# Optimization experiments

Measured on AMD Instinct MI355X. Metric: run time of the kernel, lower is better.

## Reference

```python
import jax, jax.numpy as jnp
import numpy as np

# Int8 fixed-point (power-of-two scale) quant params, mirroring Brevitas
# Int8ActPerTensorFixedPoint / Uint8ActPerTensorFixedPoint with fixed learned scales.
QMAX, QMIN, UQMAX = 127.0, -128.0, 255.0
IO_SCALE = 2.0 ** -4    # io_quant (int8) range ~ [-8, 7.94]
ACC_SCALE = 2.0 ** -3   # gate_acc_quant (int8) range ~ [-16, 15.875]
SIG_SCALE = 2.0 ** -8   # sigmoid_quant (uint8) range [0, ~0.996]
TANH_SCALE = 2.0 ** -7  # tanh_quant (int8) range ~ [-1, 0.992]


def ste_round(x):
    return x + jax.lax.stop_gradient(jnp.round(x) - x)


def qd(x, scale, qmin, qmax):
    # quantize-dequantize with straight-through rounding
    return scale * jnp.clip(ste_round(x / scale), qmin, qmax)


def quant_weight(w):
    # Int8WeightPerTensorFixedPoint: power-of-two per-tensor scale from max-abs stats
    maxabs = jax.lax.stop_gradient(jnp.max(jnp.abs(w)))
    scale = jax.lax.stop_gradient(2.0 ** jnp.ceil(jnp.log2(maxabs / QMAX)))
    return qd(w, scale, QMIN, QMAX)


def setup_inputs() -> dict:
    key = jax.random.key(0)
    ks = jax.random.split(key, 8)
    B, S, V, E, H, O = 64, 512, 32000, 512, 512, 2
    return {
        "text": jax.random.randint(ks[0], (B, S), 0, V, dtype=jnp.int32),
        "text_lengths": jax.random.randint(ks[1], (B,), 1, S, dtype=jnp.int32),
        "emb_w": jax.random.normal(ks[2], (V, E), jnp.float32) * 0.05,
        "w_ih": jax.random.normal(ks[3], (4 * H, E), jnp.float32) * 0.05,
        "w_hh": jax.random.normal(ks[4], (4 * H, H), jnp.float32) * 0.05,
        "b_ih": jax.random.normal(ks[5], (4 * H,), jnp.float32) * 0.05,
        "b_hh": jax.random.normal(ks[6], (4 * H,), jnp.float32) * 0.05,
        "fc_w": jax.random.normal(ks[7], (O, H), jnp.float32) * 0.05,
    }


def reference(text, text_lengths, emb_w, w_ih, w_hh, b_ih, b_hh, fc_w):
    B = text.shape[0]
    H = w_hh.shape[1]

    # quantized embedding lookup + io quant on LSTM input
    x = quant_weight(emb_w)[text]               # [B,S,E]
    x = qd(x, IO_SCALE, QMIN, QMAX)

    wih_q = quant_weight(w_ih)
    whh_q = quant_weight(w_hh)

    # precompute input contribution to gates: [B,S,4H]
    xg = jnp.einsum("bse,ge->bsg", x, wih_q) + b_ih + b_hh

    def step(carry, xg_t):
        h, c = carry
        gates = qd(xg_t + h @ whh_q.T, ACC_SCALE, QMIN, QMAX)  # gate_acc quant
        i, f, g, o = jnp.split(gates, 4, axis=-1)
        i = qd(jax.nn.sigmoid(i), SIG_SCALE, 0.0, UQMAX)
        f = qd(jax.nn.sigmoid(f), SIG_SCALE, 0.0, UQMAX)
        o = qd(jax.nn.sigmoid(o), SIG_SCALE, 0.0, UQMAX)
        g = qd(jnp.tanh(g), TANH_SCALE, QMIN, QMAX)
        c = f * c + i * g
        h = qd(o * qd(jnp.tanh(c), TANH_SCALE, QMIN, QMAX), IO_SCALE, QMIN, QMAX)
        return (h, c), h

    h0 = jnp.zeros((B, H), x.dtype)
    (hT, cT), _ = jax.lax.scan(step, (h0, h0), jnp.swapaxes(xg, 0, 1))

    hidden_state = hT[None]                     # [1,B,H] like torch LSTM
    return hidden_state @ quant_weight(fc_w).T  # [1,B,O]
```

## Files before the change

### kernel.cpp

```cpp
#include <hip/hip_runtime.h>
#include <math.h>

#define S_LEN  512
#define BATCH  64
#define E_DIM  512
#define H_DIM  512
#define G4     2048
#define VOCAB  32000
#define NWG    16

typedef int v4i __attribute__((ext_vector_type(4)));
typedef unsigned long long u64;

#define O_BAR   0
#define O_MAX   256
#define O_H8    512
#define O_FC8   131584
#define O_WIH8  132608
#define O_WHH8  (O_WIH8 + 1048576)
#define O_X8    (O_WHH8 + 1048576)

__device__ __forceinline__ float clampf(float x, float lo, float hi) {
    return fminf(fmaxf(x, lo), hi);
}

__device__ __forceinline__ int scale_exp(float maxabs) {
    double t = (double)maxabs / 127.0;
    int e; double f = frexp(t, &e);
    return (f == 0.5) ? (e - 1) : e;
}

__device__ __forceinline__ float xla_tanhf(float x) {
    if (fabsf(x) < 0.0004f) return x;
    float xc = fminf(fmaxf(x, -7.90531110763549805f), 7.90531110763549805f);
    float x2 = __fmul_rn(xc, xc);
    float p = fmaf(x2, -2.76076847742355e-16f, 2.00018790482477e-13f);
    p = fmaf(x2, p, -8.60467152213735e-11f);
    p = fmaf(x2, p, 5.12229709037114e-08f);
    p = fmaf(x2, p, 1.48572235717979e-05f);
    p = fmaf(x2, p, 6.37261928875436e-04f);
    p = fmaf(x2, p, 4.89352455891786e-03f);
    p = __fmul_rn(xc, p);
    float q = fmaf(x2, 1.19825839466702e-06f, 1.18534705686654e-04f);
    q = fmaf(x2, q, 2.26843463243900e-03f);
    q = fmaf(x2, q, 4.89352518554385e-03f);
    return __fdiv_rn(p, q);
}

__global__ void k_maxabs(const float* __restrict__ x, int n, unsigned* __restrict__ out) {
    unsigned m = 0;
    for (int i = blockIdx.x * blockDim.x + threadIdx.x; i < n; i += gridDim.x * blockDim.x)
        m = max(m, __float_as_uint(fabsf(x[i])));
    #pragma unroll
    for (int o = 32; o > 0; o >>= 1) {
        unsigned other = (unsigned)__shfl_down((int)m, o, 64);
        m = max(m, other);
    }
    __shared__ unsigned sm[4];
    if ((threadIdx.x & 63) == 0) sm[threadIdx.x >> 6] = m;
    __syncthreads();
    if (threadIdx.x == 0) {
        unsigned r = sm[0];
        for (int w = 1; w < (int)(blockDim.x >> 6); w++) r = max(r, sm[w]);
        atomicMax(out, r);
    }
}

__global__ void k_quantw(const float* __restrict__ w, int n, const unsigned* __restrict__ mx,
                         signed char* __restrict__ q) {
    float inv = ldexpf(1.0f, -scale_exp(__uint_as_float(*mx)));
    for (int i = blockIdx.x * blockDim.x + threadIdx.x; i < n; i += gridDim.x * blockDim.x) {
        float v = clampf(rintf(w[i] * inv), -128.0f, 127.0f);
        q[i] = (signed char)(int)v;
    }
}

__global__ void k_embed(const float* __restrict__ emb, const int* __restrict__ text,
                        const unsigned* __restrict__ mx, signed char* __restrict__ x8) {
    int row = blockIdx.x;
    int b = row >> 9, s = row & 511;
    int tok = text[row];
    int ke = scale_exp(__uint_as_float(*mx));
    float inv = ldexpf(1.0f, -ke);
    float sc2 = ldexpf(1.0f, ke + 4);
    const float4* src = (const float4*)(emb + (size_t)tok * E_DIM);
    char4* dst = (char4*)(x8 + (size_t)(s * BATCH + b) * E_DIM);
    float4 v = src[threadIdx.x];
    char4 c;
    float q;
    q = clampf(rintf(v.x * inv), -128.f, 127.f); c.x = (signed char)(int)clampf(rintf(q * sc2), -128.f, 127.f);
    q = clampf(rintf(v.y * inv), -128.f, 127.f); c.y = (signed char)(int)clampf(rintf(q * sc2), -128.f, 127.f);
    q = clampf(rintf(v.z * inv), -128.f, 127.f); c.z = (signed char)(int)clampf(rintf(q * sc2), -128.f, 127.f);
    q = clampf(rintf(v.w * inv), -128.f, 127.f); c.w = (signed char)(int)clampf(rintf(q * sc2), -128.f, 127.f);
    dst[threadIdx.x] = c;
}

#define MKFRAG(a, b) ((v4i){(a)[0], (a)[1], (b)[0], (b)[1]})

__global__ __launch_bounds__(256, 1) void k_lstm(
    const signed char* __restrict__ wih8, const signed char* __restrict__ whh8,
    const signed char* __restrict__ x8, const float* __restrict__ b_ih,
    const float* __restrict__ b_hh, const unsigned* __restrict__ mx,
    signed char* __restrict__ h8) {
    __shared__ __attribute__((aligned(16))) signed char wih_lds[128 * 528];
    __shared__ __attribute__((aligned(16))) signed char hstage[BATCH * 32];
    __shared__ float lut_sig[256];
    __shared__ float lut_tnh[256];

    const int g = blockIdx.x;
    const int tid = threadIdx.x;
    const int wv = tid >> 6, lane = tid & 63, l15 = lane & 15, qd4 = lane >> 4;
    const float sih = ldexpf(1.0f, scale_exp(__uint_as_float(mx[1])) - 4);
    const float shh = ldexpf(1.0f, scale_exp(__uint_as_float(mx[2])) - 4);

    if (tid < 256) {
        float v = (float)(tid - 128) * 0.125f;
        float sg = __fadd_rn(0.5f, __fmul_rn(0.5f, xla_tanhf(__fmul_rn(0.5f, v))));
        float sc = clampf(rintf(__fmul_rn(sg, 256.0f)), 0.0f, 255.0f);
        lut_sig[tid] = sc * 0.00390625f;
        float th = xla_tanhf(v);
        float tc = clampf(rintf(__fmul_rn(th, 128.0f)), -128.0f, 127.0f);
        lut_tnh[tid] = tc * 0.0078125f;
    }

    for (int it = 0; it < 16; it++) {
        int idx = it * 256 + tid;
        int r = idx >> 5, cc = (idx & 31) * 16;
        int grow = (r >> 5) * 512 + g * 32 + (r & 31);
        *(v4i*)(wih_lds + r * 528 + cc) = *(const v4i*)(wih8 + (size_t)grow * 512 + cc);
    }

    v4i whf[8][8];
    #pragma unroll
    for (int nt = 0; nt < 8; nt++) {
        int nl = nt * 16 + l15;
        size_t grow = (size_t)((nl >> 5) * 512 + g * 32 + (nl & 31)) * 512;
        #pragma unroll
        for (int k = 0; k < 8; k++)
            whf[nt][k] = *(const v4i*)(whh8 + grow + k * 64 + qd4 * 16);
    }
    __syncthreads();

    float bi[8], bh[8];
    #pragma unroll
    for (int nt = 0; nt < 8; nt++) {
        int nl = nt * 16 + l15;
        int col = (nl >> 5) * 512 + g * 32 + (nl & 31);
        bi[nt] = b_ih[col];
        bh[nt] = b_hh[col];
    }

    float cst[2][4];
    #pragma unroll
    for (int jh = 0; jh < 2; jh++)
        #pragma unroll
        for (int r = 0; r < 4; r++) cst[jh][r] = 0.0f;

    v4i xacc[8];
    {
        v4i xfr[8];
        const signed char* xrow = x8 + (size_t)(wv * 16 + l15) * 512 + qd4 * 16;
        #pragma unroll
        for (int k = 0; k < 8; k++) xfr[k] = *(const v4i*)(xrow + k * 64);
        #pragma unroll
        for (int nt = 0; nt < 8; nt++) {
            v4i a = (v4i){0, 0, 0, 0};
            #pragma unroll
            for (int k = 0; k < 8; k++) {
                v4i bf = *(const v4i*)(wih_lds + (nt * 16 + l15) * 528 + k * 64 + qd4 * 16);
                a = __builtin_amdgcn_mfma_i32_16x16x64_i8(xfr[k], bf, a, 0, 0, 0);
            }
            xacc[nt] = a;
        }
    }

    const int row = wv * 16 + l15;
    const int pb = tid >> 2, psub = tid & 3;
    const u64 paddr_base = (u64)(h8) + (u64)(pb * 64 + g * 4 + psub) * 16;
    const u64 caddr_base = (u64)(h8) + (u64)(row * 64 + qd4 * 2) * 16;

    for (int t = 0; t < S_LEN; t++) {
        u64 ha = caddr_base + (u64)(t & 1) * 65536;
        int tg = t;
        v4i u0,u1,u2,u3,u4,u5,u6,u7,u8,u9,u10,u11,u12,u13,u14,u15;
        for (;;) {
            asm volatile(
                "global_load_dwordx4 %0,  %16, off sc0 sc1\n\t"
                "global_load_dwordx4 %1,  %16, off offset:16 sc0 sc1\n\t"
                "global_load_dwordx4 %2,  %16, off offset:128 sc0 sc1\n\t"
                "global_load_dwordx4 %3,  %16, off offset:144 sc0 sc1\n\t"
                "global_load_dwordx4 %4,  %16, off offset:256 sc0 sc1\n\t"
                "global_load_dwordx4 %5,  %16, off offset:272 sc0 sc1\n\t"
                "global_load_dwordx4 %6,  %16, off offset:384 sc0 sc1\n\t"
                "global_load_dwordx4 %7,  %16, off offset:400 sc0 sc1\n\t"
                "global_load_dwordx4 %8,  %16, off offset:512 sc0 sc1\n\t"
                "global_load_dwordx4 %9,  %16, off offset:528 sc0 sc1\n\t"
                "global_load_dwordx4 %10, %16, off offset:640 sc0 sc1\n\t"
                "global_load_dwordx4 %11, %16, off offset:656 sc0 sc1\n\t"
                "global_load_dwordx4 %12, %16, off offset:768 sc0 sc1\n\t"
                "global_load_dwordx4 %13, %16, off offset:784 sc0 sc1\n\t"
                "global_load_dwordx4 %14, %16, off offset:896 sc0 sc1\n\t"
                "global_load_dwordx4 %15, %16, off offset:912 sc0 sc1\n\t"
                "s_waitcnt vmcnt(0)"
                : "=&v"(u0), "=&v"(u1), "=&v"(u2), "=&v"(u3),
                  "=&v"(u4), "=&v"(u5), "=&v"(u6), "=&v"(u7),
                  "=&v"(u8), "=&v"(u9), "=&v"(u10), "=&v"(u11),
                  "=&v"(u12), "=&v"(u13), "=&v"(u14), "=&v"(u15)
                : "v"(ha)
                : "memory");
            bool ok = (u0[2] == tg) & (u1[2] == tg) & (u2[2] == tg) & (u3[2] == tg)
                    & (u4[2] == tg) & (u5[2] == tg) & (u6[2] == tg) & (u7[2] == tg)
                    & (u8[2] == tg) & (u9[2] == tg) & (u10[2] == tg) & (u11[2] == tg)
                    & (u12[2] == tg) & (u13[2] == tg) & (u14[2] == tg) & (u15[2] == tg);
            if (ok) break;
            __builtin_amdgcn_s_sleep(1);
        }
        v4i afr[8];
        afr[0] = MKFRAG(u0, u1);   afr[1] = MKFRAG(u2, u3);
        afr[2] = MKFRAG(u4, u5);   afr[3] = MKFRAG(u6, u7);
        afr[4] = MKFRAG(u8, u9);   afr[5] = MKFRAG(u10, u11);
        afr[6] = MKFRAG(u12, u13); afr[7] = MKFRAG(u14, u15);

        float pre[8][4];
        #pragma unroll
        for (int nt = 0; nt < 8; nt++) {
            v4i hacc = (v4i){0, 0, 0, 0};
            #pragma unroll
            for (int k = 0; k < 8; k++)
                hacc = __builtin_amdgcn_mfma_i32_16x16x64_i8(afr[k], whf[nt][k], hacc, 0, 0, 0);
            #pragma unroll
            for (int r = 0; r < 4; r++)
                pre[nt][r] = __fadd_rn(
                    __fadd_rn(__fadd_rn(__fmul_rn((float)xacc[nt][r], sih), bi[nt]), bh[nt]),
                    __fmul_rn((float)hacc[r], shh));
        }

        #pragma unroll
        for (int jh = 0; jh < 2; jh++)
            #pragma unroll
            for (int r = 0; r < 4; r++) {
                int ii = (int)clampf(rintf(__fmul_rn(pre[0 + jh][r], 8.0f)), -128.f, 127.f) + 128;
                int fi = (int)clampf(rintf(__fmul_rn(pre[2 + jh][r], 8.0f)), -128.f, 127.f) + 128;
                int gi = (int)clampf(rintf(__fmul_rn(pre[4 + jh][r], 8.0f)), -128.f, 127.f) + 128;
                int oi = (int)clampf(rintf(__fmul_rn(pre[6 + jh][r], 8.0f)), -128.f, 127.f) + 128;
                float iq = lut_sig[ii], fq = lut_sig[fi], oq = lut_sig[oi];
                float gq = lut_tnh[gi];
                float c = __fadd_rn(__fmul_rn(fq, cst[jh][r]), __fmul_rn(iq, gq));
                cst[jh][r] = c;
                float tc32 = xla_tanhf(c);
                float tq = clampf(rintf(__fmul_rn(tc32, 128.0f)), -128.f, 127.f) * 0.0078125f;
                float hv = __fmul_rn(oq, tq);
                int hc = (int)clampf(rintf(__fmul_rn(hv, 16.0f)), -128.f, 127.f);
                int b = wv * 16 + qd4 * 4 + r;
                hstage[b * 32 + jh * 16 + l15] = (signed char)hc;
            }

        {
            u64 codes = *(const u64*)(hstage + tid * 8);
            v4i sval = (v4i){(int)(codes & 0xffffffffu), (int)(codes >> 32), t + 1, 0};
            u64 pa = paddr_base + (u64)((t + 1) & 1) * 65536;
            asm volatile("global_store_dwordx4 %0, %1, off sc0 sc1"
                         :: "v"(pa), "v"(sval) : "memory");
        }

        if (t + 1 < S_LEN) {
            v4i xfr[8];
            const signed char* xrow = x8 + (size_t)((t + 1) * BATCH + wv * 16 + l15) * 512 + qd4 * 16;
            #pragma unroll
            for (int k = 0; k < 8; k++) xfr[k] = *(const v4i*)(xrow + k * 64);
            #pragma unroll
            for (int nt = 0; nt < 8; nt++) {
                v4i a = (v4i){0, 0, 0, 0};
                #pragma unroll
                for (int k = 0; k < 8; k++) {
                    v4i bf = *(const v4i*)(wih_lds + (nt * 16 + l15) * 528 + k * 64 + qd4 * 16);
                    a = __builtin_amdgcn_mfma_i32_16x16x64_i8(xfr[k], bf, a, 0, 0, 0);
                }
                xacc[nt] = a;
            }
        }
    }
}

__global__ void k_fc(const signed char* __restrict__ h8, const signed char* __restrict__ fc8,
                     const unsigned* __restrict__ mx_fc, float* __restrict__ out) {
    int tid = threadIdx.x;
    int b = tid >> 1, o = tid & 1;
    const signed char* hp = h8 + b * 1024;
    const char4* wp = (const char4*)(fc8 + o * 512);
    int s = 0;
    for (int i = 0; i < 64; i++) {
        u64 hv = __hip_atomic_load((const u64*)(hp + i * 16), __ATOMIC_RELAXED, __HIP_MEMORY_SCOPE_AGENT);
        char4 w0 = wp[i * 2], w1 = wp[i * 2 + 1];
        signed char hb[8];
        *(u64*)hb = hv;
        s += hb[0] * w0.x + hb[1] * w0.y + hb[2] * w0.z + hb[3] * w0.w
           + hb[4] * w1.x + hb[5] * w1.y + hb[6] * w1.z + hb[7] * w1.w;
    }
    float sc = ldexpf(1.0f, scale_exp(__uint_as_float(*mx_fc)) - 4);
    out[b * 2 + o] = (float)s * sc;
}

extern "C" void kernel_launch(void* const* d_in, const int* in_sizes, int n_in,
                              void* d_out, int out_size, void* d_ws, size_t ws_size,
                              hipStream_t stream) {
    (void)in_sizes; (void)n_in; (void)out_size; (void)ws_size;
    const int*   text = (const int*)d_in[0];
    const float* emb  = (const float*)d_in[2];
    const float* w_ih = (const float*)d_in[3];
    const float* w_hh = (const float*)d_in[4];
    const float* b_ih = (const float*)d_in[5];
    const float* b_hh = (const float*)d_in[6];
    const float* fc_w = (const float*)d_in[7];

    char* ws = (char*)d_ws;
    unsigned*    mx   = (unsigned*)(ws + O_MAX);
    signed char* h8   = (signed char*)(ws + O_H8);
    signed char* fc8  = (signed char*)(ws + O_FC8);
    signed char* wih8 = (signed char*)(ws + O_WIH8);
    signed char* whh8 = (signed char*)(ws + O_WHH8);
    signed char* x8   = (signed char*)(ws + O_X8);

    hipMemsetAsync(d_ws, 0, O_H8 + 2 * 65536, stream);

    k_maxabs<<<2048, 256, 0, stream>>>(emb, VOCAB * E_DIM, mx + 0);
    k_maxabs<<<256, 256, 0, stream>>>(w_ih, G4 * E_DIM, mx + 1);
    k_maxabs<<<256, 256, 0, stream>>>(w_hh, G4 * H_DIM, mx + 2);
    k_maxabs<<<1, 256, 0, stream>>>(fc_w, 2 * H_DIM, mx + 3);

    k_quantw<<<512, 256, 0, stream>>>(w_ih, G4 * E_DIM, mx + 1, wih8);
    k_quantw<<<512, 256, 0, stream>>>(w_hh, G4 * H_DIM, mx + 2, whh8);
    k_quantw<<<2, 256, 0, stream>>>(fc_w, 2 * H_DIM, mx + 3, fc8);

    k_embed<<<BATCH * S_LEN, 128, 0, stream>>>(emb, text, mx + 0, x8);

    k_lstm<<<NWG, 256, 0, stream>>>(wih8, whh8, x8, b_ih, b_hh, mx, h8);

    k_fc<<<1, 128, 0, stream>>>(h8, fc8, mx + 3, (float*)d_out);
}
```

Before: 2.913 ms.

## Co-locate LSTM workgroups on one XCD and use XCD-scoped coherence for h exchange

Launches 256 workgroups and has them self-organize into a team of 16, preferring blocks on the same XCD as the leader, and the rest exit. When all 16 sit on one XCD, the per-step hidden-state exchange uses sc0-only loads and stores instead of system-coherent sc0 sc1, which is meant to cut cross-die latency in the serial recurrence. A timeout fallback flushes the exchange slots and reverts to full coherence, at the cost of extra launch overhead, a more complex startup handshake and reliance on XCD-local cache coherence semantics.

```diff
diff --git a/kernel.cpp b/kernel.cpp
--- a/kernel.cpp
+++ b/kernel.cpp
@@ -7,7 +7,11 @@
 #define H_DIM  512
 #define G4     2048
 #define VOCAB  32000
-#define NWG    16
+#define NWORK  16
+#define GRID_LSTM 256
+
+#define RT_1MS   100000ull
+#define RT_200US 20000ull
 
 typedef int v4i __attribute__((ext_vector_type(4)));
 typedef unsigned long long u64;
@@ -97,17 +101,118 @@
 
 #define MKFRAG(a, b) ((v4i){(a)[0], (a)[1], (b)[0], (b)[1]})
 
+#define H_POLL(FLAGS)                                                        \
+    asm volatile(                                                            \
+        "global_load_dwordx4 %0,  %16, off " FLAGS "\n\t"                    \
+        "global_load_dwordx4 %1,  %16, off offset:16 " FLAGS "\n\t"          \
+        "global_load_dwordx4 %2,  %16, off offset:128 " FLAGS "\n\t"         \
+        "global_load_dwordx4 %3,  %16, off offset:144 " FLAGS "\n\t"         \
+        "global_load_dwordx4 %4,  %16, off offset:256 " FLAGS "\n\t"         \
+        "global_load_dwordx4 %5,  %16, off offset:272 " FLAGS "\n\t"         \
+        "global_load_dwordx4 %6,  %16, off offset:384 " FLAGS "\n\t"         \
+        "global_load_dwordx4 %7,  %16, off offset:400 " FLAGS "\n\t"         \
+        "global_load_dwordx4 %8,  %16, off offset:512 " FLAGS "\n\t"         \
+        "global_load_dwordx4 %9,  %16, off offset:528 " FLAGS "\n\t"         \
+        "global_load_dwordx4 %10, %16, off offset:640 " FLAGS "\n\t"         \
+        "global_load_dwordx4 %11, %16, off offset:656 " FLAGS "\n\t"         \
+        "global_load_dwordx4 %12, %16, off offset:768 " FLAGS "\n\t"         \
+        "global_load_dwordx4 %13, %16, off offset:784 " FLAGS "\n\t"         \
+        "global_load_dwordx4 %14, %16, off offset:896 " FLAGS "\n\t"         \
+        "global_load_dwordx4 %15, %16, off offset:912 " FLAGS "\n\t"         \
+        "s_waitcnt vmcnt(0)"                                                 \
+        : "=&v"(u0), "=&v"(u1), "=&v"(u2), "=&v"(u3),                        \
+          "=&v"(u4), "=&v"(u5), "=&v"(u6), "=&v"(u7),                        \
+          "=&v"(u8), "=&v"(u9), "=&v"(u10), "=&v"(u11),                      \
+          "=&v"(u12), "=&v"(u13), "=&v"(u14), "=&v"(u15)                     \
+        : "v"(ha)                                                            \
+        : "memory")
+
+#define H_TAGOK ((u0[2] == tg) & (u1[2] == tg) & (u2[2] == tg) & (u3[2] == tg)    \
+               & (u4[2] == tg) & (u5[2] == tg) & (u6[2] == tg) & (u7[2] == tg)    \
+               & (u8[2] == tg) & (u9[2] == tg) & (u10[2] == tg) & (u11[2] == tg)  \
+               & (u12[2] == tg) & (u13[2] == tg) & (u14[2] == tg) & (u15[2] == tg))
+
 __global__ __launch_bounds__(256, 1) void k_lstm(
     const signed char* __restrict__ wih8, const signed char* __restrict__ whh8,
     const signed char* __restrict__ x8, const float* __restrict__ b_ih,
     const float* __restrict__ b_hh, const unsigned* __restrict__ mx,
-    signed char* __restrict__ h8) {
+    signed char* __restrict__ h8, unsigned* __restrict__ team) {
     __shared__ __attribute__((aligned(16))) signed char wih_lds[128 * 528];
     __shared__ __attribute__((aligned(16))) signed char hstage[BATCH * 32];
     __shared__ float lut_sig[256];
     __shared__ float lut_tnh[256];
-
-    const int g = blockIdx.x;
+    __shared__ int s_g, s_homog;
+
+    if (threadIdx.x == 0) {
+        unsigned xcd = __builtin_amdgcn_s_getreg(6164) & 0xfu;
+        __hip_atomic_fetch_or(&team[3], 1u << xcd, __ATOMIC_RELAXED, __HIP_MEMORY_SCOPE_AGENT);
+        __hip_atomic_fetch_add(&team[4], 1u, __ATOMIC_RELAXED, __HIP_MEMORY_SCOPE_AGENT);
+        int g = -1;
+        u64 t0 = __builtin_amdgcn_s_memrealtime();
+        if (blockIdx.x == 0) {
+            g = 0;
+            __hip_atomic_store(&team[8], xcd + 1u, __ATOMIC_RELEASE, __HIP_MEMORY_SCOPE_AGENT);
+            __hip_atomic_store(&team[0], xcd + 1u, __ATOMIC_RELEASE, __HIP_MEMORY_SCOPE_AGENT);
+        } else {
+            unsigned f;
+            for (;;) {
+                f = __hip_atomic_load(&team[0], __ATOMIC_ACQUIRE, __HIP_MEMORY_SCOPE_AGENT);
+                if (f) break;
+                if (__builtin_amdgcn_s_memrealtime() - t0 > RT_1MS) { f = 0xffffffffu; break; }
+                __builtin_amdgcn_s_sleep(1);
+            }
+            bool join = (f == 0xffffffffu) || (f - 1u == xcd);
+            if (!join) {
+                for (;;) {
+                    if (__hip_atomic_load(&team[1], __ATOMIC_RELAXED, __HIP_MEMORY_SCOPE_AGENT) >= 15u)
+                        break;
+                    if (__builtin_amdgcn_s_memrealtime() - t0 > RT_200US) { join = true; break; }
+                    __builtin_amdgcn_s_sleep(1);
+                }
+            }
+            if (join) {
+                unsigned s = __hip_atomic_fetch_add(&team[1], 1u, __ATOMIC_RELAXED, __HIP_MEMORY_SCOPE_AGENT);
+                if (s < 15u) {
+                    g = (int)s + 1;
+                    __hip_atomic_store(&team[8 + g], xcd + 1u, __ATOMIC_RELEASE, __HIP_MEMORY_SCOPE_AGENT);
+                }
+            }
+        }
+        int homog = 0;
+        if (g >= 0) {
+            bool full;
+            for (;;) {
+                full = true;
+                for (int i = 0; i < 16; i++)
+                    if (__hip_atomic_load(&team[8 + i], __ATOMIC_ACQUIRE, __HIP_MEMORY_SCOPE_AGENT) == 0u)
+                        { full = false; break; }
+                if (full) break;
+                if (__builtin_amdgcn_s_memrealtime() - t0 > RT_1MS) break;
+                __builtin_amdgcn_s_sleep(1);
+            }
+            if (full) {
+                while (__hip_atomic_load(&team[4], __ATOMIC_RELAXED, __HIP_MEMORY_SCOPE_AGENT) < (unsigned)GRID_LSTM) {
+                    if (__builtin_amdgcn_s_memrealtime() - t0 > RT_1MS) { full = false; break; }
+                    __builtin_amdgcn_s_sleep(1);
+                }
+            }
+            if (full) {
+                unsigned x0 = __hip_atomic_load(&team[8], __ATOMIC_RELAXED, __HIP_MEMORY_SCOPE_AGENT);
+                homog = 1;
+                for (int i = 1; i < 16; i++)
+                    if (__hip_atomic_load(&team[8 + i], __ATOMIC_RELAXED, __HIP_MEMORY_SCOPE_AGENT) != x0)
+                        homog = 0;
+                unsigned msk = __hip_atomic_load(&team[3], __ATOMIC_RELAXED, __HIP_MEMORY_SCOPE_AGENT);
+                if (__popc(msk) < 2) homog = 0;
+            }
+        }
+        s_g = g; s_homog = homog;
+    }
+    __syncthreads();
+    const int g = s_g;
+    bool fast = (s_homog != 0);
+    if (g < 0) return;
+
     const int tid = threadIdx.x;
     const int wv = tid >> 6, lane = tid & 63, l15 = lane & 15, qd4 = lane >> 4;
     const float sih = ldexpf(1.0f, scale_exp(__uint_as_float(mx[1])) - 4);
@@ -183,36 +288,24 @@
         u64 ha = caddr_base + (u64)(t & 1) * 65536;
         int tg = t;
         v4i u0,u1,u2,u3,u4,u5,u6,u7,u8,u9,u10,u11,u12,u13,u14,u15;
+        u64 tp0 = __builtin_amdgcn_s_memrealtime();
         for (;;) {
-            asm volatile(
-                "global_load_dwordx4 %0,  %16, off sc0 sc1\n\t"
-                "global_load_dwordx4 %1,  %16, off offset:16 sc0 sc1\n\t"
-                "global_load_dwordx4 %2,  %16, off offset:128 sc0 sc1\n\t"
-                "global_load_dwordx4 %3,  %16, off offset:144 sc0 sc1\n\t"
-                "global_load_dwordx4 %4,  %16, off offset:256 sc0 sc1\n\t"
-                "global_load_dwordx4 %5,  %16, off offset:272 sc0 sc1\n\t"
-                "global_load_dwordx4 %6,  %16, off offset:384 sc0 sc1\n\t"
-                "global_load_dwordx4 %7,  %16, off offset:400 sc0 sc1\n\t"
-                "global_load_dwordx4 %8,  %16, off offset:512 sc0 sc1\n\t"
-                "global_load_dwordx4 %9,  %16, off offset:528 sc0 sc1\n\t"
-                "global_load_dwordx4 %10, %16, off offset:640 sc0 sc1\n\t"
-                "global_load_dwordx4 %11, %16, off offset:656 sc0 sc1\n\t"
-                "global_load_dwordx4 %12, %16, off offset:768 sc0 sc1\n\t"
-                "global_load_dwordx4 %13, %16, off offset:784 sc0 sc1\n\t"
-                "global_load_dwordx4 %14, %16, off offset:896 sc0 sc1\n\t"
-                "global_load_dwordx4 %15, %16, off offset:912 sc0 sc1\n\t"
-                "s_waitcnt vmcnt(0)"
-                : "=&v"(u0), "=&v"(u1), "=&v"(u2), "=&v"(u3),
-                  "=&v"(u4), "=&v"(u5), "=&v"(u6), "=&v"(u7),
-                  "=&v"(u8), "=&v"(u9), "=&v"(u10), "=&v"(u11),
-                  "=&v"(u12), "=&v"(u13), "=&v"(u14), "=&v"(u15)
-                : "v"(ha)
-                : "memory");
-            bool ok = (u0[2] == tg) & (u1[2] == tg) & (u2[2] == tg) & (u3[2] == tg)
-                    & (u4[2] == tg) & (u5[2] == tg) & (u6[2] == tg) & (u7[2] == tg)
-                    & (u8[2] == tg) & (u9[2] == tg) & (u10[2] == tg) & (u11[2] == tg)
-                    & (u12[2] == tg) & (u13[2] == tg) & (u14[2] == tg) & (u15[2] == tg);
-            if (ok) break;
+            if (fast) { H_POLL("sc0"); }
+            else      { H_POLL("sc0 sc1"); }
+            if (H_TAGOK) break;
+            if (fast && (__builtin_amdgcn_s_memrealtime() - tp0 > RT_200US)) {
+                fast = false;
+                #pragma unroll
+                for (int sl = 0; sl < 2; sl++) {
+                    u64 pa = paddr_base + (u64)sl * 65536;
+                    v4i val;
+                    asm volatile("global_load_dwordx4 %0, %1, off sc0\n\t"
+                                 "s_waitcnt vmcnt(0)"
+                                 : "=&v"(val) : "v"(pa) : "memory");
+                    asm volatile("global_store_dwordx4 %0, %1, off sc0 sc1"
+                                 :: "v"(pa), "v"(val) : "memory");
+                }
+            }
             __builtin_amdgcn_s_sleep(1);
         }
         v4i afr[8];
@@ -259,8 +352,12 @@
             u64 codes = *(const u64*)(hstage + tid * 8);
             v4i sval = (v4i){(int)(codes & 0xffffffffu), (int)(codes >> 32), t + 1, 0};
             u64 pa = paddr_base + (u64)((t + 1) & 1) * 65536;
-            asm volatile("global_store_dwordx4 %0, %1, off sc0 sc1"
-                         :: "v"(pa), "v"(sval) : "memory");
+            if (fast)
+                asm volatile("global_store_dwordx4 %0, %1, off sc0"
+                             :: "v"(pa), "v"(sval) : "memory");
+            else
+                asm volatile("global_store_dwordx4 %0, %1, off sc0 sc1"
+                             :: "v"(pa), "v"(sval) : "memory");
         }
 
         if (t + 1 < S_LEN) {
@@ -314,6 +411,7 @@
     const float* fc_w = (const float*)d_in[7];
 
     char* ws = (char*)d_ws;
+    unsigned*    team = (unsigned*)(ws + O_BAR);
     unsigned*    mx   = (unsigned*)(ws + O_MAX);
     signed char* h8   = (signed char*)(ws + O_H8);
     signed char* fc8  = (signed char*)(ws + O_FC8);
@@ -334,7 +432,7 @@
 
     k_embed<<<BATCH * S_LEN, 128, 0, stream>>>(emb, text, mx + 0, x8);
 
-    k_lstm<<<NWG, 256, 0, stream>>>(wih8, whh8, x8, b_ih, b_hh, mx, h8);
+    k_lstm<<<GRID_LSTM, 256, 0, stream>>>(wih8, whh8, x8, b_ih, b_hh, mx, h8, team);
 
     k_fc<<<1, 128, 0, stream>>>(h8, fc8, mx + 3, (float*)d_out);
 }
```

Measured after the change: 7.172 ms. 146% more time.

## Replicate hidden-state exchange buffers and move x-projection off the critical path

Applied to the files above, without the earlier changes.

Each workgroup now writes its tagged hidden-state slice to up to 16 replica buffers, and each consumer polls its own replica. This spreads the polling traffic across different memory addresses instead of having all 16 workgroups hit one buffer. The input-gate MFMA for step t+1 is also moved from after the h store to after the poll, so only the x-row load is prefetched while waiting. The cost is extra stores per step, more workspace, and a replica count that depends on the workspace size.

```diff
diff --git a/kernel.cpp b/kernel.cpp
--- a/kernel.cpp
+++ b/kernel.cpp
@@ -12,13 +12,13 @@
 typedef int v4i __attribute__((ext_vector_type(4)));
 typedef unsigned long long u64;
 
-#define O_BAR   0
-#define O_MAX   256
-#define O_H8    512
-#define O_FC8   131584
-#define O_WIH8  132608
+#define O_MAX   0
+#define O_FC8   256
+#define O_H0    2048
+#define O_WIH8  (O_H0 + 131072)
 #define O_WHH8  (O_WIH8 + 1048576)
 #define O_X8    (O_WHH8 + 1048576)
+#define O_HX    (O_X8 + S_LEN * BATCH * E_DIM)
 
 __device__ __forceinline__ float clampf(float x, float lo, float hi) {
     return fminf(fmaxf(x, lo), hi);
@@ -97,11 +97,42 @@
 
 #define MKFRAG(a, b) ((v4i){(a)[0], (a)[1], (b)[0], (b)[1]})
 
+#define H_POLL                                                               \
+    asm volatile(                                                            \
+        "global_load_dwordx4 %0,  %16, off sc0 sc1\n\t"                      \
+        "global_load_dwordx4 %1,  %16, off offset:16 sc0 sc1\n\t"            \
+        "global_load_dwordx4 %2,  %16, off offset:128 sc0 sc1\n\t"           \
+        "global_load_dwordx4 %3,  %16, off offset:144 sc0 sc1\n\t"           \
+        "global_load_dwordx4 %4,  %16, off offset:256 sc0 sc1\n\t"           \
+        "global_load_dwordx4 %5,  %16, off offset:272 sc0 sc1\n\t"           \
+        "global_load_dwordx4 %6,  %16, off offset:384 sc0 sc1\n\t"           \
+        "global_load_dwordx4 %7,  %16, off offset:400 sc0 sc1\n\t"           \
+        "global_load_dwordx4 %8,  %16, off offset:512 sc0 sc1\n\t"           \
+        "global_load_dwordx4 %9,  %16, off offset:528 sc0 sc1\n\t"           \
+        "global_load_dwordx4 %10, %16, off offset:640 sc0 sc1\n\t"           \
+        "global_load_dwordx4 %11, %16, off offset:656 sc0 sc1\n\t"           \
+        "global_load_dwordx4 %12, %16, off offset:768 sc0 sc1\n\t"           \
+        "global_load_dwordx4 %13, %16, off offset:784 sc0 sc1\n\t"           \
+        "global_load_dwordx4 %14, %16, off offset:896 sc0 sc1\n\t"           \
+        "global_load_dwordx4 %15, %16, off offset:912 sc0 sc1\n\t"           \
+        "s_waitcnt vmcnt(0)"                                                 \
+        : "=&v"(u0), "=&v"(u1), "=&v"(u2), "=&v"(u3),                        \
+          "=&v"(u4), "=&v"(u5), "=&v"(u6), "=&v"(u7),                        \
+          "=&v"(u8), "=&v"(u9), "=&v"(u10), "=&v"(u11),                      \
+          "=&v"(u12), "=&v"(u13), "=&v"(u14), "=&v"(u15)                     \
+        : "v"(ha)                                                            \
+        : "memory")
+
+#define H_TAGOK ((u0[2] == tg) & (u1[2] == tg) & (u2[2] == tg) & (u3[2] == tg)    \
+               & (u4[2] == tg) & (u5[2] == tg) & (u6[2] == tg) & (u7[2] == tg)    \
+               & (u8[2] == tg) & (u9[2] == tg) & (u10[2] == tg) & (u11[2] == tg)  \
+               & (u12[2] == tg) & (u13[2] == tg) & (u14[2] == tg) & (u15[2] == tg))
+
 __global__ __launch_bounds__(256, 1) void k_lstm(
     const signed char* __restrict__ wih8, const signed char* __restrict__ whh8,
     const signed char* __restrict__ x8, const float* __restrict__ b_ih,
     const float* __restrict__ b_hh, const unsigned* __restrict__ mx,
-    signed char* __restrict__ h8) {
+    signed char* __restrict__ h0, signed char* __restrict__ hx, int nrep) {
     __shared__ __attribute__((aligned(16))) signed char wih_lds[128 * 528];
     __shared__ __attribute__((aligned(16))) signed char hstage[BATCH * 32];
     __shared__ float lut_sig[256];
@@ -158,17 +189,17 @@
 
     v4i xacc[8];
     {
-        v4i xfr[8];
+        v4i x0fr[8];
         const signed char* xrow = x8 + (size_t)(wv * 16 + l15) * 512 + qd4 * 16;
         #pragma unroll
-        for (int k = 0; k < 8; k++) xfr[k] = *(const v4i*)(xrow + k * 64);
+        for (int k = 0; k < 8; k++) x0fr[k] = *(const v4i*)(xrow + k * 64);
         #pragma unroll
         for (int nt = 0; nt < 8; nt++) {
             v4i a = (v4i){0, 0, 0, 0};
             #pragma unroll
             for (int k = 0; k < 8; k++) {
                 v4i bf = *(const v4i*)(wih_lds + (nt * 16 + l15) * 528 + k * 64 + qd4 * 16);
-                a = __builtin_amdgcn_mfma_i32_16x16x64_i8(xfr[k], bf, a, 0, 0, 0);
+                a = __builtin_amdgcn_mfma_i32_16x16x64_i8(x0fr[k], bf, a, 0, 0, 0);
             }
             xacc[nt] = a;
         }
@@ -176,43 +207,22 @@
 
     const int row = wv * 16 + l15;
     const int pb = tid >> 2, psub = tid & 3;
-    const u64 paddr_base = (u64)(h8) + (u64)(pb * 64 + g * 4 + psub) * 16;
-    const u64 caddr_base = (u64)(h8) + (u64)(row * 64 + qd4 * 2) * 16;
+    const u64 unit_off = (u64)(pb * 64 + g * 4 + psub) * 16;
+    const u64 p0_base = (u64)(h0) + unit_off;
+    const u64 px_base = (u64)(hx) + unit_off;
+    const int myc = g & (nrep - 1);
+    const u64 cb = myc ? ((u64)(hx) + (u64)(myc - 1) * 131072) : (u64)(h0);
+    const u64 caddr_base = cb + (u64)(row * 64 + qd4 * 2) * 16;
+
+    v4i xfr[8];
 
     for (int t = 0; t < S_LEN; t++) {
         u64 ha = caddr_base + (u64)(t & 1) * 65536;
         int tg = t;
         v4i u0,u1,u2,u3,u4,u5,u6,u7,u8,u9,u10,u11,u12,u13,u14,u15;
         for (;;) {
-            asm volatile(
-                "global_load_dwordx4 %0,  %16, off sc0 sc1\n\t"
-                "global_load_dwordx4 %1,  %16, off offset:16 sc0 sc1\n\t"
-                "global_load_dwordx4 %2,  %16, off offset:128 sc0 sc1\n\t"
-                "global_load_dwordx4 %3,  %16, off offset:144 sc0 sc1\n\t"
-                "global_load_dwordx4 %4,  %16, off offset:256 sc0 sc1\n\t"
-                "global_load_dwordx4 %5,  %16, off offset:272 sc0 sc1\n\t"
-                "global_load_dwordx4 %6,  %16, off offset:384 sc0 sc1\n\t"
-                "global_load_dwordx4 %7,  %16, off offset:400 sc0 sc1\n\t"
-                "global_load_dwordx4 %8,  %16, off offset:512 sc0 sc1\n\t"
-                "global_load_dwordx4 %9,  %16, off offset:528 sc0 sc1\n\t"
-                "global_load_dwordx4 %10, %16, off offset:640 sc0 sc1\n\t"
-                "global_load_dwordx4 %11, %16, off offset:656 sc0 sc1\n\t"
-                "global_load_dwordx4 %12, %16, off offset:768 sc0 sc1\n\t"
-                "global_load_dwordx4 %13, %16, off offset:784 sc0 sc1\n\t"
-                "global_load_dwordx4 %14, %16, off offset:896 sc0 sc1\n\t"
-                "global_load_dwordx4 %15, %16, off offset:912 sc0 sc1\n\t"
-                "s_waitcnt vmcnt(0)"
-                : "=&v"(u0), "=&v"(u1), "=&v"(u2), "=&v"(u3),
-                  "=&v"(u4), "=&v"(u5), "=&v"(u6), "=&v"(u7),
-                  "=&v"(u8), "=&v"(u9), "=&v"(u10), "=&v"(u11),
-                  "=&v"(u12), "=&v"(u13), "=&v"(u14), "=&v"(u15)
-                : "v"(ha)
-                : "memory");
-            bool ok = (u0[2] == tg) & (u1[2] == tg) & (u2[2] == tg) & (u3[2] == tg)
-                    & (u4[2] == tg) & (u5[2] == tg) & (u6[2] == tg) & (u7[2] == tg)
-                    & (u8[2] == tg) & (u9[2] == tg) & (u10[2] == tg) & (u11[2] == tg)
-                    & (u12[2] == tg) & (u13[2] == tg) & (u14[2] == tg) & (u15[2] == tg);
-            if (ok) break;
+            H_POLL;
+            if (H_TAGOK) break;
             __builtin_amdgcn_s_sleep(1);
         }
         v4i afr[8];
@@ -220,6 +230,19 @@
         afr[2] = MKFRAG(u4, u5);   afr[3] = MKFRAG(u6, u7);
         afr[4] = MKFRAG(u8, u9);   afr[5] = MKFRAG(u10, u11);
         afr[6] = MKFRAG(u12, u13); afr[7] = MKFRAG(u14, u15);
+
+        if (t > 0) {
+            #pragma unroll
+            for (int nt = 0; nt < 8; nt++) {
+                v4i a = (v4i){0, 0, 0, 0};
+                #pragma unroll
+                for (int k = 0; k < 8; k++) {
+                    v4i bf = *(const v4i*)(wih_lds + (nt * 16 + l15) * 528 + k * 64 + qd4 * 16);
+                    a = __builtin_amdgcn_mfma_i32_16x16x64_i8(xfr[k], bf, a, 0, 0, 0);
+                }
+                xacc[nt] = a;
+            }
+        }
 
         float pre[8][4];
         #pragma unroll
@@ -258,26 +281,22 @@
         {
             u64 codes = *(const u64*)(hstage + tid * 8);
             v4i sval = (v4i){(int)(codes & 0xffffffffu), (int)(codes >> 32), t + 1, 0};
-            u64 pa = paddr_base + (u64)((t + 1) & 1) * 65536;
+            u64 slot = (u64)((t + 1) & 1) * 65536;
+            u64 pa = p0_base + slot;
             asm volatile("global_store_dwordx4 %0, %1, off sc0 sc1"
                          :: "v"(pa), "v"(sval) : "memory");
+            u64 px = px_base + slot;
+            for (int c = 1; c < nrep; c++) {
+                asm volatile("global_store_dwordx4 %0, %1, off sc0 sc1"
+                             :: "v"(px), "v"(sval) : "memory");
+                px += 131072;
+            }
         }
 
         if (t + 1 < S_LEN) {
-            v4i xfr[8];
             const signed char* xrow = x8 + (size_t)((t + 1) * BATCH + wv * 16 + l15) * 512 + qd4 * 16;
             #pragma unroll
             for (int k = 0; k < 8; k++) xfr[k] = *(const v4i*)(xrow + k * 64);
-            #pragma unroll
-            for (int nt = 0; nt < 8; nt++) {
-                v4i a = (v4i){0, 0, 0, 0};
-                #pragma unroll
-                for (int k = 0; k < 8; k++) {
-                    v4i bf = *(const v4i*)(wih_lds + (nt * 16 + l15) * 528 + k * 64 + qd4 * 16);
-                    a = __builtin_amdgcn_mfma_i32_16x16x64_i8(xfr[k], bf, a, 0, 0, 0);
-                }
-                xacc[nt] = a;
-            }
         }
     }
 }
@@ -304,7 +323,7 @@
 extern "C" void kernel_launch(void* const* d_in, const int* in_sizes, int n_in,
                               void* d_out, int out_size, void* d_ws, size_t ws_size,
                               hipStream_t stream) {
-    (void)in_sizes; (void)n_in; (void)out_size; (void)ws_size;
+    (void)in_sizes; (void)n_in; (void)out_size;
     const int*   text = (const int*)d_in[0];
     const float* emb  = (const float*)d_in[2];
     const float* w_ih = (const float*)d_in[3];
@@ -315,13 +334,22 @@
 
     char* ws = (char*)d_ws;
     unsigned*    mx   = (unsigned*)(ws + O_MAX);
-    signed char* h8   = (signed char*)(ws + O_H8);
     signed char* fc8  = (signed char*)(ws + O_FC8);
+    signed char* h0   = (signed char*)(ws + O_H0);
     signed char* wih8 = (signed char*)(ws + O_WIH8);
     signed char* whh8 = (signed char*)(ws + O_WHH8);
     signed char* x8   = (signed char*)(ws + O_X8);
-
-    hipMemsetAsync(d_ws, 0, O_H8 + 2 * 65536, stream);
+    signed char* hx   = (signed char*)(ws + O_HX);
+
+    size_t avail = ws_size > (size_t)O_HX ? ws_size - (size_t)O_HX : 0;
+    int extra = (int)(avail / 131072);
+    int nrep = 1;
+    while (nrep < 16 && nrep * 2 <= extra + 1) nrep *= 2;
+
+    hipMemsetAsync(ws + O_MAX, 0, 256, stream);
+    hipMemsetAsync(ws + O_H0, 0, 131072, stream);
+    if (nrep > 1)
+        hipMemsetAsync(ws + O_HX, 0, (size_t)(nrep - 1) * 131072, stream);
 
     k_maxabs<<<2048, 256, 0, stream>>>(emb, VOCAB * E_DIM, mx + 0);
     k_maxabs<<<256, 256, 0, stream>>>(w_ih, G4 * E_DIM, mx + 1);
@@ -334,7 +362,7 @@
 
     k_embed<<<BATCH * S_LEN, 128, 0, stream>>>(emb, text, mx + 0, x8);
 
-    k_lstm<<<NWG, 256, 0, stream>>>(wih8, whh8, x8, b_ih, b_hh, mx, h8);
-
-    k_fc<<<1, 128, 0, stream>>>(h8, fc8, mx + 3, (float*)d_out);
-}
+    k_lstm<<<NWG, 256, 0, stream>>>(wih8, whh8, x8, b_ih, b_hh, mx, h0, hx, nrep);
+
+    k_fc<<<1, 128, 0, stream>>>(h0, fc8, mx + 3, (float*)d_out);
+}
```

Measured after the change: 3.754 ms. 28.9% more time.
